# Kernel tuning notes

Measured on AMD Instinct MI355X. Metric: run time of the kernel, lower is better.

Reference implementation:

```python
import jax, jax.numpy as jnp
import numpy as np

B, L, DIM, H, HD = 1, 2048, 2048, 16, 128  # head_dim = DIM // H; RoPE pairs = HD // 2


def setup_inputs() -> dict:
    key = jax.random.key(0)
    ks = jax.random.split(key, 6)
    x = jax.random.normal(ks[0], (B, L, DIM), dtype=jnp.float32)
    pe = jax.random.normal(ks[1], (1, 1, L, HD // 2, 2, 2), dtype=jnp.float32)
    qkv_w = jax.random.normal(ks[2], (3 * DIM, DIM), dtype=jnp.float32) * 0.02
    q_scale = jnp.ones((HD,), dtype=jnp.float32)
    k_scale = jnp.ones((HD,), dtype=jnp.float32)
    proj_w = jax.random.normal(ks[3], (DIM, DIM), dtype=jnp.float32) * 0.02
    proj_b = jnp.zeros((DIM,), dtype=jnp.float32)
    return {"x": x, "pe": pe, "qkv_w": qkv_w, "q_scale": q_scale,
            "k_scale": k_scale, "proj_w": proj_w, "proj_b": proj_b}


def _rmsnorm(t, scale):
    # per-head-dim RMSNorm, eps=1e-6, computed in fp32 (inputs already fp32)
    rrms = jax.lax.rsqrt(jnp.mean(t * t, axis=-1, keepdims=True) + 1e-6)
    return t * rrms * scale


def _apply_rope(q, k, pe):
    def rot(t):
        t_ = t.reshape(*t.shape[:-1], -1, 1, 2)  # [B,H,L,HD/2,1,2]
        out = pe[..., 0] * t_[..., 0] + pe[..., 1] * t_[..., 1]  # [B,H,L,HD/2,2]
        return out.reshape(t.shape)
    return rot(q), rot(k)


def reference(x, pe, qkv_w, q_scale, k_scale, proj_w, proj_b):
    b, l, _ = x.shape
    qkv = jnp.einsum('bld,ed->ble', x, qkv_w)  # [B, L, 3*DIM]
    qkv = qkv.reshape(b, l, 3, H, HD)
    # 'B L (K H D) -> K B H L D'
    qkv = jnp.transpose(qkv, (2, 0, 3, 1, 4))
    q, k, v = qkv[0], qkv[1], qkv[2]  # each [B, H, L, HD]
    q = _rmsnorm(q, q_scale)
    k = _rmsnorm(k, k_scale)
    q, k = _apply_rope(q, k, pe)
    scale = 1.0 / jnp.sqrt(jnp.asarray(HD, dtype=q.dtype))
    scores = jnp.einsum('bhqd,bhkd->bhqk', q, k) * scale
    attn = jax.nn.softmax(scores, axis=-1)
    out = jnp.einsum('bhqk,bhkd->bhqd', attn, v)  # [B, H, L, HD]
    out = jnp.transpose(out, (0, 2, 1, 3)).reshape(b, l, H * HD)  # 'B H L D -> B L (H D)'
    return jnp.einsum('bld,ed->ble', out, proj_w) + proj_b
```

## Files before the change

kernel.cpp:

```cpp
#include <hip/hip_runtime.h>
#include <hip/hip_bf16.h>
#include <math.h>

#define L_SEQ 2048
#define DIM   2048
#define NH    16
#define HD    128
#define TDIM  6144

typedef __attribute__((ext_vector_type(8))) short short8;
typedef __attribute__((ext_vector_type(4))) float f32x4;
typedef __attribute__((ext_vector_type(4))) unsigned int u32x4;

__device__ __forceinline__ void gl_lds16(const void* g, void* l) {
  __builtin_amdgcn_global_load_lds(
      (const __attribute__((address_space(1))) unsigned int*)g,
      (__attribute__((address_space(3))) unsigned int*)l, 16, 0, 0);
}

__device__ __forceinline__ short bf16bits(float x) {
  __hip_bfloat16 h = __float2bfloat16(x);
  return *(short*)&h;
}

__device__ __forceinline__ float bits2f(short s) {
  unsigned int u = ((unsigned int)(unsigned short)s) << 16;
  return __uint_as_float(u);
}

__device__ __forceinline__ unsigned int pack_bf16(float a, float b) {
  __hip_bfloat162 h = __float22bfloat162_rn(make_float2(a, b));
  return *(unsigned int*)&h;
}

__global__ __launch_bounds__(256)
void cast2_bf16(const float* __restrict__ a, __hip_bfloat16* __restrict__ oa,
                const float* __restrict__ b, __hip_bfloat16* __restrict__ ob) {
  int i = (blockIdx.x * 256 + threadIdx.x) * 8;
  const float* src;
  __hip_bfloat16* dst;
  int off;
  if (i < DIM * DIM) { src = a; dst = oa; off = i; }
  else               { src = b; dst = ob; off = i - DIM * DIM; }
  float4 v0 = *(const float4*)(src + off);
  float4 v1 = *(const float4*)(src + off + 4);
  short8 o;
  o[0] = bf16bits(v0.x); o[1] = bf16bits(v0.y); o[2] = bf16bits(v0.z); o[3] = bf16bits(v0.w);
  o[4] = bf16bits(v1.x); o[5] = bf16bits(v1.y); o[6] = bf16bits(v1.z); o[7] = bf16bits(v1.w);
  *(short8*)(dst + off) = o;
}

__global__ __launch_bounds__(256)
void cast_bf16(const float* __restrict__ in, __hip_bfloat16* __restrict__ out, int n) {
  int i = (blockIdx.x * 256 + threadIdx.x) * 8;
  if (i >= n) return;
  float4 a = *(const float4*)(in + i);
  float4 b = *(const float4*)(in + i + 4);
  short8 o;
  o[0] = bf16bits(a.x); o[1] = bf16bits(a.y); o[2] = bf16bits(a.z); o[3] = bf16bits(a.w);
  o[4] = bf16bits(b.x); o[5] = bf16bits(b.y); o[6] = bf16bits(b.z); o[7] = bf16bits(b.w);
  *(short8*)(out + i) = o;
}

#define QKV_N 6144
#define QKV_K 2048

__global__ __launch_bounds__(512, 2)
void gemm_qkv_256(const __hip_bfloat16* __restrict__ A,
                  const __hip_bfloat16* __restrict__ B,
                  __hip_bfloat16* __restrict__ C) {
  extern __shared__ char smem[];
  const int tid  = threadIdx.x;
  const int lane = tid & 63, w = tid >> 6;
  const int l15  = lane & 15, quad = lane >> 4;
  const int wm   = w >> 2, wn = w & 3;

  const int orig = blockIdx.x;
  const int by = orig & 7;
  const int bx = orig >> 3;
  const int m0 = by * 256, n0 = bx * 256;

  const int ar0 = tid >> 2,         aq0 = tid & 3;
  const int ar1 = (512 + tid) >> 2, aq1 = (512 + tid) & 3;
  const __hip_bfloat16* pA0 = A + (size_t)(m0 + ar0) * QKV_K + aq0 * 8;
  const __hip_bfloat16* pA1 = A + (size_t)(m0 + ar1) * QKV_K + aq1 * 8;
  const __hip_bfloat16* pB0 = B + (size_t)(n0 + ar0) * QKV_K + aq0 * 8;
  const __hip_bfloat16* pB1 = B + (size_t)(n0 + ar1) * QKV_K + aq1 * 8;
  const int dst0 = w * 1024;

  f32x4 acc[8][4];
#pragma unroll
  for (int mi = 0; mi < 8; ++mi)
#pragma unroll
    for (int ni = 0; ni < 4; ++ni) acc[mi][ni] = (f32x4){0.f, 0.f, 0.f, 0.f};

  const int aoff = ((wm * 128 + l15) * 32 + quad * 8) * 2;
  const int boff = ((wn * 64 + l15) * 32 + quad * 8) * 2;

#pragma unroll
  for (int p = 0; p < 3; ++p) {
    char* Sp = smem + p * 32768;
    gl_lds16(pA0 + p * 32, Sp + dst0);
    gl_lds16(pA1 + p * 32, Sp + dst0 + 8192);
    gl_lds16(pB0 + p * 32, Sp + 16384 + dst0);
    gl_lds16(pB1 + p * 32, Sp + 16384 + dst0 + 8192);
  }
  asm volatile("s_waitcnt vmcnt(8)\n\ts_barrier" ::: "memory");

  for (int tb = 0; tb < 64; tb += 4) {
#pragma unroll
    for (int u = 0; u < 4; ++u) {
      const int t  = tb + u;
      const char* As = smem + u * 32768;
      const char* Bs = As + 16384;
      const int tn = (t + 3) & 63;
      char* Sn = smem + ((u + 3) & 3) * 32768;

      short8 a[8];
#pragma unroll
      for (int mi = 0; mi < 8; ++mi)
        a[mi] = *(const short8*)(As + aoff + mi * 1024);
      short8 b0 = *(const short8*)(Bs + boff);
      short8 b1 = *(const short8*)(Bs + boff + 1024);
      gl_lds16(pA0 + tn * 32, Sn + dst0);
      gl_lds16(pA1 + tn * 32, Sn + dst0 + 8192);
      __builtin_amdgcn_s_barrier();
      __builtin_amdgcn_s_setprio(1);
#pragma unroll
      for (int mi = 0; mi < 8; ++mi) {
        acc[mi][0] = __builtin_amdgcn_mfma_f32_16x16x32_bf16(a[mi], b0, acc[mi][0], 0, 0, 0);
        acc[mi][1] = __builtin_amdgcn_mfma_f32_16x16x32_bf16(a[mi], b1, acc[mi][1], 0, 0, 0);
      }
      __builtin_amdgcn_s_setprio(0);
      __builtin_amdgcn_s_barrier();

      short8 b2 = *(const short8*)(Bs + boff + 2048);
      short8 b3 = *(const short8*)(Bs + boff + 3072);
      gl_lds16(pB0 + tn * 32, Sn + 16384 + dst0);
      gl_lds16(pB1 + tn * 32, Sn + 16384 + dst0 + 8192);
      asm volatile("s_waitcnt vmcnt(8)\n\ts_barrier" ::: "memory");
      __builtin_amdgcn_s_setprio(1);
#pragma unroll
      for (int mi = 0; mi < 8; ++mi) {
        acc[mi][2] = __builtin_amdgcn_mfma_f32_16x16x32_bf16(a[mi], b2, acc[mi][2], 0, 0, 0);
        acc[mi][3] = __builtin_amdgcn_mfma_f32_16x16x32_bf16(a[mi], b3, acc[mi][3], 0, 0, 0);
      }
      __builtin_amdgcn_s_setprio(0);
      __builtin_amdgcn_s_barrier();
    }
  }

  const int crow = m0 + wm * 128 + quad * 4;
  const int ccol = n0 + wn * 64 + l15;
#pragma unroll
  for (int mi = 0; mi < 8; ++mi)
#pragma unroll
    for (int ni = 0; ni < 4; ++ni)
#pragma unroll
      for (int r = 0; r < 4; ++r)
        C[(size_t)(crow + mi * 16 + r) * QKV_N + ccol + ni * 16] =
            __float2bfloat16(acc[mi][ni][r]);
}

__global__ __launch_bounds__(256)
void qkv_epilogue(const __hip_bfloat16* __restrict__ C,
                  const float* __restrict__ q_scale, const float* __restrict__ k_scale,
                  const float* __restrict__ pe,
                  __hip_bfloat16* __restrict__ Qb, __hip_bfloat16* __restrict__ Kb,
                  __hip_bfloat16* __restrict__ Vt) {
  const int bid = blockIdx.x;
  const int t = threadIdx.x;
  if (bid < 512) {
    const int sec = bid >> 8;
    const int h   = (bid >> 4) & 15;
    const int rb  = bid & 15;
    const float* scale = sec ? k_scale : q_scale;
    const float qmul = sec ? 1.0f : 0.08838834764831845f;
    __hip_bfloat16* dst = sec ? Kb : Qb;

    const int row = t >> 1, half = t & 1;
    const int l = rb * 128 + row;
    const __hip_bfloat16* grow = C + (size_t)l * TDIM + sec * DIM + h * HD + half * 64;

    float ss = 0.f;
#pragma unroll
    for (int c8 = 0; c8 < 64; c8 += 8) {
      short8 v8 = *(const short8*)(grow + c8);
#pragma unroll
      for (int j = 0; j < 8; ++j) { float f = bits2f(v8[j]); ss += f * f; }
    }
    ss += __shfl_xor(ss, 1);
    const float rrms = rsqrtf(ss * (1.f / 128.f) + 1e-6f);

    const float* perow = pe + (size_t)l * 256 + half * 128;
    __hip_bfloat16* drow = dst + ((size_t)h * L_SEQ + l) * HD + half * 64;

#pragma unroll
    for (int c8 = 0; c8 < 64; c8 += 8) {
      short8 v8 = *(const short8*)(grow + c8);
      float f[8];
#pragma unroll
      for (int j = 0; j < 8; ++j)
        f[j] = bits2f(v8[j]) * rrms * scale[half * 64 + c8 + j];
      short8 o;
#pragma unroll
      for (int p = 0; p < 4; ++p) {
        float4 pp = *(const float4*)(perow + c8 * 2 + p * 4);
        float e = f[2 * p], od = f[2 * p + 1];
        o[2 * p]     = bf16bits((pp.x * e + pp.y * od) * qmul);
        o[2 * p + 1] = bf16bits((pp.z * e + pp.w * od) * qmul);
      }
      *(short8*)(drow + c8) = o;
    }
  } else {
    __shared__ short Tt[128 * 72];
    const int vb = bid - 512;
    const int h = vb >> 5, lb = vb & 31;
    const int l0 = lb * 64;
#pragma unroll
    for (int k = 0; k < 4; ++k) {
      int idx = t + k * 256;
      int row = idx >> 4, c = idx & 15;
      short8 v = *(const short8*)(C + (size_t)(l0 + row) * TDIM + 2 * DIM + h * HD + c * 8);
#pragma unroll
      for (int j = 0; j < 8; ++j) Tt[(c * 8 + j) * 72 + row] = v[j];
    }
    __syncthreads();
    const int d = t >> 1, lh = t & 1;
    __hip_bfloat16* vrow = Vt + ((size_t)h * HD + d) * L_SEQ + l0 + lh * 32;
#pragma unroll
    for (int k = 0; k < 4; ++k) {
      short8 o = *(const short8*)&Tt[d * 72 + lh * 32 + k * 8];
      *(short8*)(vrow + k * 8) = o;
    }
  }
}

__global__ __launch_bounds__(256)
void gemm_proj(const __hip_bfloat16* __restrict__ A, const __hip_bfloat16* __restrict__ B,
               const float* __restrict__ bias, float* __restrict__ C,
               int M, int N, int K) {
  const int n0 = blockIdx.x * 128, m0 = blockIdx.y * 128;
  const int t = threadIdx.x, lane = t & 63, w = t >> 6;
  const int l15 = lane & 15, quad = lane >> 4;
  const int wm = (w & 1) * 64, wn = (w >> 1) * 64;

  __shared__ __align__(16) __hip_bfloat16 As[128 * 32];
  __shared__ __align__(16) __hip_bfloat16 Bs[128 * 32];

  f32x4 acc[4][4];
#pragma unroll
  for (int mt = 0; mt < 4; ++mt)
#pragma unroll
    for (int nt = 0; nt < 4; ++nt) acc[mt][nt] = (f32x4){0.f, 0.f, 0.f, 0.f};

  const int arow  = lane >> 2;
  const int acol8 = (lane & 3) * 8;
  const __hip_bfloat16* Ab = A + (size_t)(m0 + w * 16 + arow) * K + acol8;
  const __hip_bfloat16* Bb = B + (size_t)(n0 + w * 16 + arow) * K + acol8;
  __hip_bfloat16* As_base = As + (size_t)(w * 16) * 32;
  __hip_bfloat16* Bs_base = Bs + (size_t)(w * 16) * 32;

  for (int kb = 0; kb < K; kb += 32) {
    gl_lds16(Ab + kb,                As_base);
    gl_lds16(Ab + kb + (size_t)64*K, As_base + 64 * 32);
    gl_lds16(Bb + kb,                Bs_base);
    gl_lds16(Bb + kb + (size_t)64*K, Bs_base + 64 * 32);
    __syncthreads();

    short8 am[4], bn[4];
#pragma unroll
    for (int mt = 0; mt < 4; ++mt)
      am[mt] = *(const short8*)&As[(size_t)(wm + mt*16 + l15) * 32 + quad * 8];
#pragma unroll
    for (int nt = 0; nt < 4; ++nt)
      bn[nt] = *(const short8*)&Bs[(size_t)(wn + nt*16 + l15) * 32 + quad * 8];
#pragma unroll
    for (int mt = 0; mt < 4; ++mt)
#pragma unroll
      for (int nt = 0; nt < 4; ++nt)
        acc[mt][nt] = __builtin_amdgcn_mfma_f32_16x16x32_bf16(am[mt], bn[nt], acc[mt][nt], 0, 0, 0);
    __syncthreads();
  }

#pragma unroll
  for (int mt = 0; mt < 4; ++mt)
#pragma unroll
    for (int nt = 0; nt < 4; ++nt) {
      int col = n0 + wn + nt * 16 + l15;
#pragma unroll
      for (int r = 0; r < 4; ++r) {
        int row = m0 + wm + mt * 16 + quad * 4 + r;
        C[(size_t)row * N + col] = acc[mt][nt][r] + bias[col];
      }
    }
}

__global__ __launch_bounds__(256, 4)
void attn_mfma(const __hip_bfloat16* __restrict__ Qb,
               const __hip_bfloat16* __restrict__ Kb,
               const __hip_bfloat16* __restrict__ Vt,
               __hip_bfloat16* __restrict__ Opart, float2* __restrict__ ml) {
  const int q0 = blockIdx.x * 64;
  const int h  = blockIdx.y;
  const int z  = blockIdx.z;
  const int t  = threadIdx.x;
  const int lane = t & 63, w = t >> 6;
  const int l15 = lane & 15, quad = lane >> 4;
  const int sw = l15 & 7;

  __shared__ __align__(16) __hip_bfloat16 Ks[64 * 128];
  __shared__ __align__(16) __hip_bfloat16 Vs[128 * 64];

  const __hip_bfloat16* kbase = Kb + (size_t)h * L_SEQ * HD;
  const __hip_bfloat16* vbase = Vt + (size_t)h * HD * L_SEQ;

  short8 aq[4];
  {
    const __hip_bfloat16* qbase = Qb + ((size_t)h * L_SEQ + q0 + w * 16 + l15) * HD;
#pragma unroll
    for (int ks = 0; ks < 4; ++ks)
      aq[ks] = *(const short8*)(qbase + ks * 32 + quad * 8);
  }

  f32x4 o[8];
#pragma unroll
  for (int n2 = 0; n2 < 8; ++n2) o[n2] = (f32x4){0.f, 0.f, 0.f, 0.f};
  float m_run = -1e30f, l_run = 0.f;

  for (int kt = 0; kt < 16; ++kt) {
    const int k0 = z * (L_SEQ / 2) + kt * 64;
#pragma unroll
    for (int i = 0; i < 4; ++i) {
      int krow = w * 16 + i * 4 + (lane >> 4);
      int kch  = (lane & 15) ^ (krow & 7);
      gl_lds16(kbase + (size_t)(k0 + krow) * HD + kch * 8,
               &Ks[(w * 16 + i * 4) * 128]);
    }
#pragma unroll
    for (int i = 0; i < 4; ++i) {
      int vrow = w * 32 + i * 8 + (lane >> 3);
      int vch  = (lane & 7) ^ (vrow & 7);
      gl_lds16(vbase + (size_t)vrow * L_SEQ + k0 + vch * 8,
               &Vs[(w * 32 + i * 8) * 64]);
    }
    __syncthreads();

    f32x4 s[4];
#pragma unroll
    for (int nt = 0; nt < 4; ++nt) s[nt] = (f32x4){0.f, 0.f, 0.f, 0.f};
#pragma unroll
    for (int ks = 0; ks < 4; ++ks) {
      short8 bk[4];
#pragma unroll
      for (int nt = 0; nt < 4; ++nt)
        bk[nt] = *(const short8*)&Ks[(nt * 16 + l15) * 128 + ((ks * 4 + quad) ^ sw) * 8];
#pragma unroll
      for (int nt = 0; nt < 4; ++nt)
        s[nt] = __builtin_amdgcn_mfma_f32_16x16x32_bf16(bk[nt], aq[ks], s[nt], 0, 0, 0);
    }

    float mx0 = fmaxf(fmaxf(s[0][0], s[0][1]), fmaxf(s[0][2], s[0][3]));
    float mx1 = fmaxf(fmaxf(s[1][0], s[1][1]), fmaxf(s[1][2], s[1][3]));
    float mx2 = fmaxf(fmaxf(s[2][0], s[2][1]), fmaxf(s[2][2], s[2][3]));
    float mx3 = fmaxf(fmaxf(s[3][0], s[3][1]), fmaxf(s[3][2], s[3][3]));
    float rm = fmaxf(fmaxf(mx0, mx1), fmaxf(mx2, mx3));
    rm = fmaxf(rm, __shfl_xor(rm, 16));
    rm = fmaxf(rm, __shfl_xor(rm, 32));
    float mnew = fmaxf(m_run, rm);
    float alpha = __expf(m_run - mnew);
    m_run = mnew;

    float sum = 0.f;
#pragma unroll
    for (int nt = 0; nt < 4; ++nt)
#pragma unroll
      for (int r = 0; r < 4; ++r) {
        float p = __expf(s[nt][r] - mnew);
        s[nt][r] = p;
        sum += p;
      }
    sum += __shfl_xor(sum, 16);
    sum += __shfl_xor(sum, 32);
    l_run = l_run * alpha + sum;

    float alpha_r[4];
#pragma unroll
    for (int r = 0; r < 4; ++r) alpha_r[r] = __shfl(alpha, quad * 4 + r);
#pragma unroll
    for (int n2 = 0; n2 < 8; ++n2)
#pragma unroll
      for (int r = 0; r < 4; ++r) o[n2][r] *= alpha_r[r];

    unsigned int pk[4][2];
#pragma unroll
    for (int nt = 0; nt < 4; ++nt) {
      pk[nt][0] = pack_bf16(s[nt][0], s[nt][1]);
      pk[nt][1] = pack_bf16(s[nt][2], s[nt][3]);
    }
    short8 ap[2];
#pragma unroll
    for (int ks2 = 0; ks2 < 2; ++ks2) {
      u32x4 a32;
#pragma unroll
      for (int jp = 0; jp < 4; ++jp) {
        int quad_src = (quad & 1) * 2 + (jp >> 1);
        int src = (quad_src << 4) | l15;
        int rp = jp & 1;
        unsigned int v0 = __shfl((int)pk[2 * ks2 + 0][rp], src);
        unsigned int v1 = __shfl((int)pk[2 * ks2 + 1][rp], src);
        a32[jp] = (quad >> 1) ? v1 : v0;
      }
      ap[ks2] = *(short8*)&a32;
    }

#pragma unroll
    for (int ks2 = 0; ks2 < 2; ++ks2)
#pragma unroll
      for (int n2 = 0; n2 < 8; ++n2) {
        short8 bv = *(const short8*)&Vs[(n2 * 16 + l15) * 64 + ((ks2 * 4 + quad) ^ sw) * 8];
        o[n2] = __builtin_amdgcn_mfma_f32_16x16x32_bf16(ap[ks2], bv, o[n2], 0, 0, 0);
      }

    __syncthreads();
  }

  const size_t rb = (size_t)(z * NH + h) * L_SEQ + q0 + w * 16;
  float linv[4];
#pragma unroll
  for (int r = 0; r < 4; ++r) linv[r] = 1.f / __shfl(l_run, quad * 4 + r);
#pragma unroll
  for (int r = 0; r < 4; ++r) {
    size_t row = rb + quad * 4 + r;
#pragma unroll
    for (int n2 = 0; n2 < 8; ++n2)
      Opart[row * HD + n2 * 16 + l15] = __float2bfloat16(o[n2][r] * linv[r]);
  }
  if (quad == 0) ml[rb + l15] = make_float2(m_run, l_run);
}

__global__ __launch_bounds__(256)
void attn_combine(const __hip_bfloat16* __restrict__ Opart,
                  const float2* __restrict__ ml,
                  __hip_bfloat16* __restrict__ out) {
  const int h  = blockIdx.y;
  const int q  = blockIdx.x * 16 + (threadIdx.x >> 4);
  const int d8 = (threadIdx.x & 15) * 8;
  const size_t i0 = (size_t)h * L_SEQ + q;
  const size_t i1 = (size_t)(NH + h) * L_SEQ + q;
  float2 a = ml[i0], b = ml[i1];
  float M  = fmaxf(a.x, b.x);
  float w1 = __expf(a.x - M) * a.y;
  float w2 = __expf(b.x - M) * b.y;
  float inv = 1.f / (w1 + w2);
  w1 *= inv; w2 *= inv;
  short8 o1 = *(const short8*)&Opart[i0 * HD + d8];
  short8 o2 = *(const short8*)&Opart[i1 * HD + d8];
  short8 r;
#pragma unroll
  for (int j = 0; j < 8; ++j)
    r[j] = bf16bits(w1 * bits2f(o1[j]) + w2 * bits2f(o2[j]));
  *(short8*)&out[(size_t)q * DIM + h * HD + d8] = r;
}

extern "C" void kernel_launch(void* const* d_in, const int* in_sizes, int n_in,
                              void* d_out, int out_size, void* d_ws, size_t ws_size,
                              hipStream_t stream) {
  const float* x       = (const float*)d_in[0];
  const float* pe      = (const float*)d_in[1];
  const float* qkv_w   = (const float*)d_in[2];
  const float* q_scale = (const float*)d_in[3];
  const float* k_scale = (const float*)d_in[4];
  const float* proj_w  = (const float*)d_in[5];
  const float* proj_b  = (const float*)d_in[6];
  float* out = (float*)d_out;

  char* base = (char*)d_ws;
  __hip_bfloat16* xb       = (__hip_bfloat16*)base;
  __hip_bfloat16* wb       = (__hip_bfloat16*)(base + 8388608);
  __hip_bfloat16* Cq       = (__hip_bfloat16*)(base + 33554432);
  __hip_bfloat16* pwb      = (__hip_bfloat16*)(base + 58720256);
  __hip_bfloat16* Qb       = (__hip_bfloat16*)base;
  __hip_bfloat16* Kb       = (__hip_bfloat16*)(base + 8388608);
  __hip_bfloat16* Vt       = (__hip_bfloat16*)(base + 16777216);
  __hip_bfloat16* Opart    = (__hip_bfloat16*)(base + 33554432);
  float2*         ml       = (float2*)(base + 50331648);
  __hip_bfloat16* attn_out = (__hip_bfloat16*)(base + 25165824);

  static bool attr_done = false;
  if (!attr_done) {
    hipFuncSetAttribute((const void*)gemm_qkv_256,
                        hipFuncAttributeMaxDynamicSharedMemorySize, 131072);
    attr_done = true;
  }

  cast2_bf16<<<dim3((DIM * DIM + TDIM * DIM) / (256 * 8)), 256, 0, stream>>>(
      x, xb, qkv_w, wb);

  gemm_qkv_256<<<dim3((TDIM / 256) * (L_SEQ / 256)), 512, 131072, stream>>>(xb, wb, Cq);

  qkv_epilogue<<<dim3(1024), 256, 0, stream>>>(Cq, q_scale, k_scale, pe, Qb, Kb, Vt);

  cast_bf16<<<dim3(DIM * DIM / (256 * 8)), 256, 0, stream>>>(proj_w, pwb, DIM * DIM);

  attn_mfma<<<dim3(L_SEQ / 64, NH, 2), 256, 0, stream>>>(Qb, Kb, Vt, Opart, ml);
  attn_combine<<<dim3(L_SEQ / 16, NH), 256, 0, stream>>>(Opart, ml, attn_out);

  gemm_proj<<<dim3(DIM / 128, DIM / 128), 256, 0, stream>>>(
      attn_out, pwb, proj_b, out, L_SEQ, DIM, DIM);
}
```

Before: 329.5 us.

## Drop attention split-K, double-buffer K/V loads, remap blocks for XCD locality

The attention kernel no longer splits the key range across two blocks. Each block now walks all 32 key tiles and writes normalized output directly, so the combine kernel and the partial-output buffers go away. K/V tiles are double-buffered in LDS, with the next tile's load issued before the current tile's compute, and MFMA sections run at raised wave priority. A 1-D grid is swizzled so that blocks of the same head land together (likely per-XCD). In exchange the grid halves to 512 blocks, which lowers parallelism, and LDS use doubles, which cuts occupancy.

```diff
diff --git a/kernel.cpp b/kernel.cpp
--- a/kernel.cpp
+++ b/kernel.cpp
@@ -296,24 +296,43 @@
     }
 }
 
-__global__ __launch_bounds__(256, 4)
+__global__ __launch_bounds__(256, 2)
 void attn_mfma(const __hip_bfloat16* __restrict__ Qb,
                const __hip_bfloat16* __restrict__ Kb,
                const __hip_bfloat16* __restrict__ Vt,
-               __hip_bfloat16* __restrict__ Opart, float2* __restrict__ ml) {
-  const int q0 = blockIdx.x * 64;
-  const int h  = blockIdx.y;
-  const int z  = blockIdx.z;
+               __hip_bfloat16* __restrict__ out) {
+  const int orig = blockIdx.x;
+  const int wg   = (orig & 7) * 64 + (orig >> 3);
+  const int h    = wg >> 5;
+  const int q0   = (wg & 31) * 64;
   const int t  = threadIdx.x;
   const int lane = t & 63, w = t >> 6;
   const int l15 = lane & 15, quad = lane >> 4;
   const int sw = l15 & 7;
 
-  __shared__ __align__(16) __hip_bfloat16 Ks[64 * 128];
-  __shared__ __align__(16) __hip_bfloat16 Vs[128 * 64];
+  __shared__ __align__(16) __hip_bfloat16 Ks[2][64 * 128];
+  __shared__ __align__(16) __hip_bfloat16 Vs[2][128 * 64];
 
   const __hip_bfloat16* kbase = Kb + (size_t)h * L_SEQ * HD;
   const __hip_bfloat16* vbase = Vt + (size_t)h * HD * L_SEQ;
+
+  auto STAGE = [&](int kt_, int b_) {
+    const int k0_ = kt_ * 64;
+#pragma unroll
+    for (int i = 0; i < 4; ++i) {
+      int krow = w * 16 + i * 4 + (lane >> 4);
+      int kch  = (lane & 15) ^ (krow & 7);
+      gl_lds16(kbase + (size_t)(k0_ + krow) * HD + kch * 8,
+               &Ks[b_][(w * 16 + i * 4) * 128]);
+    }
+#pragma unroll
+    for (int i = 0; i < 4; ++i) {
+      int vrow = w * 32 + i * 8 + (lane >> 3);
+      int vch  = (lane & 7) ^ (vrow & 7);
+      gl_lds16(vbase + (size_t)vrow * L_SEQ + k0_ + vch * 8,
+               &Vs[b_][(w * 32 + i * 8) * 64]);
+    }
+  };
 
   short8 aq[4];
   {
@@ -328,37 +347,28 @@
   for (int n2 = 0; n2 < 8; ++n2) o[n2] = (f32x4){0.f, 0.f, 0.f, 0.f};
   float m_run = -1e30f, l_run = 0.f;
 
-  for (int kt = 0; kt < 16; ++kt) {
-    const int k0 = z * (L_SEQ / 2) + kt * 64;
-#pragma unroll
-    for (int i = 0; i < 4; ++i) {
-      int krow = w * 16 + i * 4 + (lane >> 4);
-      int kch  = (lane & 15) ^ (krow & 7);
-      gl_lds16(kbase + (size_t)(k0 + krow) * HD + kch * 8,
-               &Ks[(w * 16 + i * 4) * 128]);
-    }
-#pragma unroll
-    for (int i = 0; i < 4; ++i) {
-      int vrow = w * 32 + i * 8 + (lane >> 3);
-      int vch  = (lane & 7) ^ (vrow & 7);
-      gl_lds16(vbase + (size_t)vrow * L_SEQ + k0 + vch * 8,
-               &Vs[(w * 32 + i * 8) * 64]);
-    }
-    __syncthreads();
+  STAGE(0, 0);
+  asm volatile("s_waitcnt vmcnt(0)\n\ts_barrier" ::: "memory");
+
+  for (int kt = 0; kt < 32; ++kt) {
+    const int buf = kt & 1;
+    if (kt < 31) STAGE(kt + 1, buf ^ 1);
 
     f32x4 s[4];
 #pragma unroll
     for (int nt = 0; nt < 4; ++nt) s[nt] = (f32x4){0.f, 0.f, 0.f, 0.f};
+    __builtin_amdgcn_s_setprio(1);
 #pragma unroll
     for (int ks = 0; ks < 4; ++ks) {
       short8 bk[4];
 #pragma unroll
       for (int nt = 0; nt < 4; ++nt)
-        bk[nt] = *(const short8*)&Ks[(nt * 16 + l15) * 128 + ((ks * 4 + quad) ^ sw) * 8];
+        bk[nt] = *(const short8*)&Ks[buf][(nt * 16 + l15) * 128 + ((ks * 4 + quad) ^ sw) * 8];
 #pragma unroll
       for (int nt = 0; nt < 4; ++nt)
         s[nt] = __builtin_amdgcn_mfma_f32_16x16x32_bf16(bk[nt], aq[ks], s[nt], 0, 0, 0);
     }
+    __builtin_amdgcn_s_setprio(0);
 
     float mx0 = fmaxf(fmaxf(s[0][0], s[0][1]), fmaxf(s[0][2], s[0][3]));
     float mx1 = fmaxf(fmaxf(s[1][0], s[1][1]), fmaxf(s[1][2], s[1][3]));
@@ -414,53 +424,30 @@
       ap[ks2] = *(short8*)&a32;
     }
 
+    __builtin_amdgcn_s_setprio(1);
 #pragma unroll
     for (int ks2 = 0; ks2 < 2; ++ks2)
 #pragma unroll
       for (int n2 = 0; n2 < 8; ++n2) {
-        short8 bv = *(const short8*)&Vs[(n2 * 16 + l15) * 64 + ((ks2 * 4 + quad) ^ sw) * 8];
+        short8 bv = *(const short8*)&Vs[buf][(n2 * 16 + l15) * 64 + ((ks2 * 4 + quad) ^ sw) * 8];
         o[n2] = __builtin_amdgcn_mfma_f32_16x16x32_bf16(ap[ks2], bv, o[n2], 0, 0, 0);
       }
-
-    __syncthreads();
-  }
-
-  const size_t rb = (size_t)(z * NH + h) * L_SEQ + q0 + w * 16;
+    __builtin_amdgcn_s_setprio(0);
+
+    asm volatile("s_waitcnt vmcnt(0)\n\ts_barrier" ::: "memory");
+  }
+
   float linv[4];
 #pragma unroll
   for (int r = 0; r < 4; ++r) linv[r] = 1.f / __shfl(l_run, quad * 4 + r);
 #pragma unroll
   for (int r = 0; r < 4; ++r) {
-    size_t row = rb + quad * 4 + r;
+    int row = q0 + w * 16 + quad * 4 + r;
 #pragma unroll
     for (int n2 = 0; n2 < 8; ++n2)
-      Opart[row * HD + n2 * 16 + l15] = __float2bfloat16(o[n2][r] * linv[r]);
-  }
-  if (quad == 0) ml[rb + l15] = make_float2(m_run, l_run);
-}
-
-__global__ __launch_bounds__(256)
-void attn_combine(const __hip_bfloat16* __restrict__ Opart,
-                  const float2* __restrict__ ml,
-                  __hip_bfloat16* __restrict__ out) {
-  const int h  = blockIdx.y;
-  const int q  = blockIdx.x * 16 + (threadIdx.x >> 4);
-  const int d8 = (threadIdx.x & 15) * 8;
-  const size_t i0 = (size_t)h * L_SEQ + q;
-  const size_t i1 = (size_t)(NH + h) * L_SEQ + q;
-  float2 a = ml[i0], b = ml[i1];
-  float M  = fmaxf(a.x, b.x);
-  float w1 = __expf(a.x - M) * a.y;
-  float w2 = __expf(b.x - M) * b.y;
-  float inv = 1.f / (w1 + w2);
-  w1 *= inv; w2 *= inv;
-  short8 o1 = *(const short8*)&Opart[i0 * HD + d8];
-  short8 o2 = *(const short8*)&Opart[i1 * HD + d8];
-  short8 r;
-#pragma unroll
-  for (int j = 0; j < 8; ++j)
-    r[j] = bf16bits(w1 * bits2f(o1[j]) + w2 * bits2f(o2[j]));
-  *(short8*)&out[(size_t)q * DIM + h * HD + d8] = r;
+      out[(size_t)row * DIM + h * HD + n2 * 16 + l15] =
+          __float2bfloat16(o[n2][r] * linv[r]);
+  }
 }
 
 extern "C" void kernel_launch(void* const* d_in, const int* in_sizes, int n_in,
@@ -483,8 +470,6 @@
   __hip_bfloat16* Qb       = (__hip_bfloat16*)base;
   __hip_bfloat16* Kb       = (__hip_bfloat16*)(base + 8388608);
   __hip_bfloat16* Vt       = (__hip_bfloat16*)(base + 16777216);
-  __hip_bfloat16* Opart    = (__hip_bfloat16*)(base + 33554432);
-  float2*         ml       = (float2*)(base + 50331648);
   __hip_bfloat16* attn_out = (__hip_bfloat16*)(base + 25165824);
 
   static bool attr_done = false;
@@ -503,8 +488,7 @@
 
   cast_bf16<<<dim3(DIM * DIM / (256 * 8)), 256, 0, stream>>>(proj_w, pwb, DIM * DIM);
 
-  attn_mfma<<<dim3(L_SEQ / 64, NH, 2), 256, 0, stream>>>(Qb, Kb, Vt, Opart, ml);
-  attn_combine<<<dim3(L_SEQ / 16, NH), 256, 0, stream>>>(Opart, ml, attn_out);
+  attn_mfma<<<dim3(512), 256, 0, stream>>>(Qb, Kb, Vt, attn_out);
 
   gemm_proj<<<dim3(DIM / 128, DIM / 128), 256, 0, stream>>>(
       attn_out, pwb, proj_b, out, L_SEQ, DIM, DIM);
```

After: 329.3 us. No clear change (-0.0%).

## Split attention KV into four chunks with XCD-aware grid remap and lazy rescale

Applied to the files above, without the earlier changes.

Attention now splits the key sequence into four partitions instead of two, which doubles the block count to spread work across more CUs. It uses a 1D grid remapped so that consecutive blocks on each XCD share a head, for L2 reuse. It adds s_setprio around the MFMA sections and skips the online-softmax rescale unless the running max grows by more than 8. Workspace buffers are rearranged so the larger Opart fits, and the combine kernel merges four partials. The costs are more partial-output traffic and combine work, plus slightly different numerics from the thresholded rescale.

```diff
diff --git a/kernel.cpp b/kernel.cpp
--- a/kernel.cpp
+++ b/kernel.cpp
@@ -296,14 +296,20 @@
     }
 }
 
+#define NZ 4
+#define ZLEN (L_SEQ / NZ)
+
 __global__ __launch_bounds__(256, 4)
 void attn_mfma(const __hip_bfloat16* __restrict__ Qb,
                const __hip_bfloat16* __restrict__ Kb,
                const __hip_bfloat16* __restrict__ Vt,
                __hip_bfloat16* __restrict__ Opart, float2* __restrict__ ml) {
-  const int q0 = blockIdx.x * 64;
-  const int h  = blockIdx.y;
-  const int z  = blockIdx.z;
+  const int orig = blockIdx.x;
+  const int wg   = (orig & 7) * 256 + (orig >> 3);
+  const int h    = wg >> 7;
+  const int rem  = wg & 127;
+  const int z    = rem >> 5;
+  const int q0   = (rem & 31) * 64;
   const int t  = threadIdx.x;
   const int lane = t & 63, w = t >> 6;
   const int l15 = lane & 15, quad = lane >> 4;
@@ -328,8 +334,8 @@
   for (int n2 = 0; n2 < 8; ++n2) o[n2] = (f32x4){0.f, 0.f, 0.f, 0.f};
   float m_run = -1e30f, l_run = 0.f;
 
-  for (int kt = 0; kt < 16; ++kt) {
-    const int k0 = z * (L_SEQ / 2) + kt * 64;
+  for (int kt = 0; kt < ZLEN / 64; ++kt) {
+    const int k0 = z * ZLEN + kt * 64;
 #pragma unroll
     for (int i = 0; i < 4; ++i) {
       int krow = w * 16 + i * 4 + (lane >> 4);
@@ -349,6 +355,7 @@
     f32x4 s[4];
 #pragma unroll
     for (int nt = 0; nt < 4; ++nt) s[nt] = (f32x4){0.f, 0.f, 0.f, 0.f};
+    __builtin_amdgcn_s_setprio(1);
 #pragma unroll
     for (int ks = 0; ks < 4; ++ks) {
       short8 bk[4];
@@ -359,6 +366,7 @@
       for (int nt = 0; nt < 4; ++nt)
         s[nt] = __builtin_amdgcn_mfma_f32_16x16x32_bf16(bk[nt], aq[ks], s[nt], 0, 0, 0);
     }
+    __builtin_amdgcn_s_setprio(0);
 
     float mx0 = fmaxf(fmaxf(s[0][0], s[0][1]), fmaxf(s[0][2], s[0][3]));
     float mx1 = fmaxf(fmaxf(s[1][0], s[1][1]), fmaxf(s[1][2], s[1][3]));
@@ -367,30 +375,33 @@
     float rm = fmaxf(fmaxf(mx0, mx1), fmaxf(mx2, mx3));
     rm = fmaxf(rm, __shfl_xor(rm, 16));
     rm = fmaxf(rm, __shfl_xor(rm, 32));
-    float mnew = fmaxf(m_run, rm);
-    float alpha = __expf(m_run - mnew);
-    m_run = mnew;
+
+    if (!__all(rm <= m_run + 8.f)) {
+      float mnew = fmaxf(m_run, rm);
+      float alpha = __expf(m_run - mnew);
+      m_run = mnew;
+      l_run *= alpha;
+      float alpha_r[4];
+#pragma unroll
+      for (int r = 0; r < 4; ++r) alpha_r[r] = __shfl(alpha, quad * 4 + r);
+#pragma unroll
+      for (int n2 = 0; n2 < 8; ++n2)
+#pragma unroll
+        for (int r = 0; r < 4; ++r) o[n2][r] *= alpha_r[r];
+    }
 
     float sum = 0.f;
 #pragma unroll
     for (int nt = 0; nt < 4; ++nt)
 #pragma unroll
       for (int r = 0; r < 4; ++r) {
-        float p = __expf(s[nt][r] - mnew);
+        float p = __expf(s[nt][r] - m_run);
         s[nt][r] = p;
         sum += p;
       }
     sum += __shfl_xor(sum, 16);
     sum += __shfl_xor(sum, 32);
-    l_run = l_run * alpha + sum;
-
-    float alpha_r[4];
-#pragma unroll
-    for (int r = 0; r < 4; ++r) alpha_r[r] = __shfl(alpha, quad * 4 + r);
-#pragma unroll
-    for (int n2 = 0; n2 < 8; ++n2)
-#pragma unroll
-      for (int r = 0; r < 4; ++r) o[n2][r] *= alpha_r[r];
+    l_run += sum;
 
     unsigned int pk[4][2];
 #pragma unroll
@@ -414,6 +425,7 @@
       ap[ks2] = *(short8*)&a32;
     }
 
+    __builtin_amdgcn_s_setprio(1);
 #pragma unroll
     for (int ks2 = 0; ks2 < 2; ++ks2)
 #pragma unroll
@@ -421,6 +433,7 @@
         short8 bv = *(const short8*)&Vs[(n2 * 16 + l15) * 64 + ((ks2 * 4 + quad) ^ sw) * 8];
         o[n2] = __builtin_amdgcn_mfma_f32_16x16x32_bf16(ap[ks2], bv, o[n2], 0, 0, 0);
       }
+    __builtin_amdgcn_s_setprio(0);
 
     __syncthreads();
   }
@@ -440,26 +453,38 @@
 }
 
 __global__ __launch_bounds__(256)
-void attn_combine(const __hip_bfloat16* __restrict__ Opart,
-                  const float2* __restrict__ ml,
-                  __hip_bfloat16* __restrict__ out) {
+void attn_combine4(const __hip_bfloat16* __restrict__ Opart,
+                   const float2* __restrict__ ml,
+                   __hip_bfloat16* __restrict__ out) {
   const int h  = blockIdx.y;
   const int q  = blockIdx.x * 16 + (threadIdx.x >> 4);
   const int d8 = (threadIdx.x & 15) * 8;
-  const size_t i0 = (size_t)h * L_SEQ + q;
-  const size_t i1 = (size_t)(NH + h) * L_SEQ + q;
-  float2 a = ml[i0], b = ml[i1];
-  float M  = fmaxf(a.x, b.x);
-  float w1 = __expf(a.x - M) * a.y;
-  float w2 = __expf(b.x - M) * b.y;
-  float inv = 1.f / (w1 + w2);
-  w1 *= inv; w2 *= inv;
-  short8 o1 = *(const short8*)&Opart[i0 * HD + d8];
-  short8 o2 = *(const short8*)&Opart[i1 * HD + d8];
+  size_t idx[NZ];
+  float2 a[NZ];
+#pragma unroll
+  for (int zz = 0; zz < NZ; ++zz) {
+    idx[zz] = ((size_t)zz * NH + h) * L_SEQ + q;
+    a[zz] = ml[idx[zz]];
+  }
+  float M = fmaxf(fmaxf(a[0].x, a[1].x), fmaxf(a[2].x, a[3].x));
+  float wz[NZ];
+  float tot = 0.f;
+#pragma unroll
+  for (int zz = 0; zz < NZ; ++zz) {
+    wz[zz] = __expf(a[zz].x - M) * a[zz].y;
+    tot += wz[zz];
+  }
+  float inv = 1.f / tot;
+  float acc[8] = {0.f, 0.f, 0.f, 0.f, 0.f, 0.f, 0.f, 0.f};
+#pragma unroll
+  for (int zz = 0; zz < NZ; ++zz) {
+    short8 ov = *(const short8*)&Opart[idx[zz] * HD + d8];
+#pragma unroll
+    for (int j = 0; j < 8; ++j) acc[j] += wz[zz] * bits2f(ov[j]);
+  }
   short8 r;
 #pragma unroll
-  for (int j = 0; j < 8; ++j)
-    r[j] = bf16bits(w1 * bits2f(o1[j]) + w2 * bits2f(o2[j]));
+  for (int j = 0; j < 8; ++j) r[j] = bf16bits(acc[j] * inv);
   *(short8*)&out[(size_t)q * DIM + h * HD + d8] = r;
 }
 
@@ -479,13 +504,13 @@
   __hip_bfloat16* xb       = (__hip_bfloat16*)base;
   __hip_bfloat16* wb       = (__hip_bfloat16*)(base + 8388608);
   __hip_bfloat16* Cq       = (__hip_bfloat16*)(base + 33554432);
-  __hip_bfloat16* pwb      = (__hip_bfloat16*)(base + 58720256);
   __hip_bfloat16* Qb       = (__hip_bfloat16*)base;
   __hip_bfloat16* Kb       = (__hip_bfloat16*)(base + 8388608);
   __hip_bfloat16* Vt       = (__hip_bfloat16*)(base + 16777216);
   __hip_bfloat16* Opart    = (__hip_bfloat16*)(base + 33554432);
-  float2*         ml       = (float2*)(base + 50331648);
-  __hip_bfloat16* attn_out = (__hip_bfloat16*)(base + 25165824);
+  float2*         ml       = (float2*)(base + 25165824);
+  __hip_bfloat16* attn_out = (__hip_bfloat16*)base;
+  __hip_bfloat16* pwb      = (__hip_bfloat16*)(base + 33554432);
 
   static bool attr_done = false;
   if (!attr_done) {
@@ -501,10 +526,11 @@
 
   qkv_epilogue<<<dim3(1024), 256, 0, stream>>>(Cq, q_scale, k_scale, pe, Qb, Kb, Vt);
 
+  attn_mfma<<<dim3(NZ * NH * (L_SEQ / 64)), 256, 0, stream>>>(Qb, Kb, Vt, Opart, ml);
+
+  attn_combine4<<<dim3(L_SEQ / 16, NH), 256, 0, stream>>>(Opart, ml, attn_out);
+
   cast_bf16<<<dim3(DIM * DIM / (256 * 8)), 256, 0, stream>>>(proj_w, pwb, DIM * DIM);
-
-  attn_mfma<<<dim3(L_SEQ / 64, NH, 2), 256, 0, stream>>>(Qb, Kb, Vt, Opart, ml);
-  attn_combine<<<dim3(L_SEQ / 16, NH), 256, 0, stream>>>(Opart, ml, attn_out);
 
   gemm_proj<<<dim3(DIM / 128, DIM / 128), 256, 0, stream>>>(
       attn_out, pwb, proj_b, out, L_SEQ, DIM, DIM);
```

Result: no change. 329.1 us (-0.1%).
